# Kernel optimization log

Hardware: AMD Instinct MI355X
Metric: run time of the kernel (lower is better)

The kernel has to match this reference:

```python
import jax, jax.numpy as jnp
import numpy as np

B, S, H = 2, 2048, 2048
NH, NKV, HD = 16, 8, 128        # head_dim = H // NH
WINDOW = 1024                    # sliding window size
THETA = 100000.0                 # rope_theta (RotaryEmbedding base)


def setup_inputs() -> dict:
    key = jax.random.key(0)
    ks = jax.random.split(key, 5)
    hidden = jax.random.normal(ks[0], (B, S, H), jnp.float32)
    # fused QKV projection: [H, NH*HD + 2*NKV*HD]
    W_pack = jax.random.normal(ks[1], (H, NH * HD + 2 * NKV * HD), jnp.float32) * (H ** -0.5)
    W_o = jax.random.normal(ks[2], (NH * HD, H), jnp.float32) * ((NH * HD) ** -0.5)
    # per-KV-head 2-tap causal conv weights, softmax-normalized (as in nn.Parameter init)
    conv_k = jax.nn.softmax(jax.random.normal(ks[3], (NKV, 2), jnp.float32), axis=-1)
    conv_v = jax.nn.softmax(jax.random.normal(ks[4], (NKV, 2), jnp.float32), axis=-1)
    return {"hidden": hidden, "W_pack": W_pack, "W_o": W_o, "conv_k": conv_k, "conv_v": conv_v}


def _rope(x, cos, sin):
    # x: (b, s, h, d); cos/sin: (s, d//2); non-interleaved (rotate-half) form
    d2 = x.shape[-1] // 2
    x1, x2 = x[..., :d2], x[..., d2:]
    c = cos[None, :, None, :]
    s = sin[None, :, None, :]
    return jnp.concatenate([x1 * c - x2 * s, x2 * c + x1 * s], axis=-1)


def _causal_conv2(x, w):
    # x: (b, s, kv, d); w: (kv, 2). out[t] = w0*x[t-1] + w1*x[t], zero-padded at t=0
    x_prev = jnp.pad(x, ((0, 0), (1, 0), (0, 0), (0, 0)))[:, :-1]
    return w[None, None, :, 0:1] * x_prev + w[None, None, :, 1:2] * x


def reference(hidden, W_pack, W_o, conv_k, conv_v):
    b, s, _ = hidden.shape
    qkv = hidden @ W_pack                                  # (b, s, NH*HD + 2*NKV*HD)
    q = qkv[..., : NH * HD].reshape(b, s, NH, HD)
    k = qkv[..., NH * HD : NH * HD + NKV * HD].reshape(b, s, NKV, HD)
    v = qkv[..., NH * HD + NKV * HD :].reshape(b, s, NKV, HD)

    inv_freq = 1.0 / (THETA ** (jnp.arange(0, HD, 2, dtype=jnp.float32) / HD))
    freqs = jnp.outer(jnp.arange(s, dtype=jnp.float32), inv_freq)  # (s, HD/2)
    cos, sin = jnp.cos(freqs), jnp.sin(freqs)
    q = _rope(q, cos, sin)
    k = _rope(k, cos, sin)

    # learned 2-tap causal conv mixing adjacent K/V states, per KV head
    k = _causal_conv2(k, conv_k)
    v = _causal_conv2(v, conv_v)

    # GQA: repeat kv heads to match query heads
    group = NH // NKV
    k = jnp.repeat(k, group, axis=2)  # (b, s, NH, HD)
    v = jnp.repeat(v, group, axis=2)

    scores = jnp.einsum('bqhd,bkhd->bhqk', q, k) / jnp.sqrt(jnp.float32(HD))
    i = jnp.arange(s)[:, None]
    j = jnp.arange(s)[None, :]
    mask = (j <= i) & (i - j < WINDOW)  # causal sliding-window mask
    scores = jnp.where(mask[None, None], scores, jnp.finfo(scores.dtype).min)
    probs = jax.nn.softmax(scores, axis=-1)
    out = jnp.einsum('bhqk,bkhd->bqhd', probs, v).reshape(b, s, NH * HD)
    return out @ W_o
```

## Files before the change

### kernel.cpp

```cpp
#include <hip/hip_runtime.h>

#define DI __device__ __forceinline__

typedef unsigned short u16;
typedef __attribute__((ext_vector_type(8))) short s16x8;
typedef __attribute__((ext_vector_type(8))) unsigned short u16x8;
typedef __attribute__((ext_vector_type(4))) float f32x4;
typedef __attribute__((ext_vector_type(16))) float f32x16;

DI u16 f2bf(float x) {
  union { float f; unsigned u; } a; a.f = x;
  unsigned r = a.u + 0x7FFFu + ((a.u >> 16) & 1u);
  return (u16)(r >> 16);
}
DI float bf2f(u16 u) {
  union { unsigned u; float f; } a; a.u = ((unsigned)u) << 16;
  return a.f;
}
DI void gload16(const void* g, void* l) {
  __builtin_amdgcn_global_load_lds(
      (const __attribute__((address_space(1))) unsigned int*)g,
      (__attribute__((address_space(3))) unsigned int*)l, 16, 0, 0);
}
DI f32x4 mfma16(s16x8 a, s16x8 b, f32x4 c) {
  return __builtin_amdgcn_mfma_f32_16x16x32_bf16(a, b, c, 0, 0, 0);
}
DI f32x16 mfma32(s16x8 a, s16x8 b, f32x16 c) {
  return __builtin_amdgcn_mfma_f32_32x32x16_bf16(a, b, c, 0, 0, 0);
}

DI void store_out(float* p, float v) { *p = v; }
DI void store_out(u16* p, float v) { *p = f2bf(v); }

#define SBAR() asm volatile("s_barrier" ::: "memory")
#define WAIT_LGKM0() do { asm volatile("s_waitcnt lgkmcnt(0)" ::: "memory"); \
                          __builtin_amdgcn_sched_barrier(0); } while (0)

__global__ void cvt_kernel(const float* __restrict__ in, u16* __restrict__ out, int n8) {
  int i = blockIdx.x * 256 + threadIdx.x;
  if (i >= n8) return;
  const float4* p = (const float4*)in + (size_t)i * 2;
  float4 a = p[0], b = p[1];
  u16x8 o;
  o[0] = f2bf(a.x); o[1] = f2bf(a.y); o[2] = f2bf(a.z); o[3] = f2bf(a.w);
  o[4] = f2bf(b.x); o[5] = f2bf(b.y); o[6] = f2bf(b.z); o[7] = f2bf(b.w);
  *((u16x8*)out + i) = o;
}

__global__ void cvt_t_kernel(const float* __restrict__ W, u16* __restrict__ Wt, int R, int C) {
  __shared__ u16 tile[64][65];
  int c0 = blockIdx.x * 64, r0 = blockIdx.y * 64;
  int t = threadIdx.x;
#pragma unroll
  for (int i = 0; i < 16; ++i) {
    int flat = i * 256 + t;
    int r = flat >> 6, c = flat & 63;
    tile[r][c] = f2bf(W[(size_t)(r0 + r) * C + (c0 + c)]);
  }
  __syncthreads();
#pragma unroll
  for (int i = 0; i < 16; ++i) {
    int flat = i * 256 + t;
    int c = flat >> 6, r = flat & 63;
    Wt[(size_t)(c0 + c) * R + (r0 + r)] = tile[r][c];
  }
}

__global__ void rope_table_kernel(float* __restrict__ cosT, float* __restrict__ sinT) {
  int i = blockIdx.x * 256 + threadIdx.x;
  int s = i >> 6, d = i & 63;
  float inv = expf(-(float)d * (11.5129254649702295f / 64.f));
  float f = (float)s * inv;
  cosT[i] = cosf(f);
  sinT[i] = sinf(f);
}

template <typename OutT>
__global__ __launch_bounds__(512, 2) void gemm8p_kernel(
    const u16* __restrict__ A, const u16* __restrict__ Bt, OutT* __restrict__ C,
    int M, int N, int K) {
  __shared__ __align__(16) char lds[131072];
  int nwg = gridDim.x;
  int bid = blockIdx.x;
  int cpx = nwg >> 3;
  int swz = (bid & 7) * cpx + (bid >> 3);
  int ntn = N >> 8;
  int bm = swz / ntn, bn = swz - bm * ntn;
  int m0 = bm << 8, n0 = bn << 8;
  int t = threadIdx.x, w = t >> 6, l = t & 63;
  int wm = w >> 2, wn = w & 3;
  int NT = K >> 6;

  unsigned offA[2][2], offB[2][2];
  int cA[2][2], cB[2][2];
#pragma unroll
  for (int h = 0; h < 2; ++h)
#pragma unroll
    for (int i = 0; i < 2; ++i) {
      int c = i * 16 + h * 8 + w;
      cA[h][i] = c;
      int d = c * 1024 + l * 16;
      int s = d ^ (((d >> 9) & 1) << 5);
      offA[h][i] = (unsigned)(m0 + (s >> 7)) * (unsigned)(K * 2) + (unsigned)(s & 127);
      int c2 = ((w >> 2) << 3) + (w & 3) + h * 4 + i * 16;
      cB[h][i] = c2;
      int d2 = c2 * 1024 + l * 16;
      int s2 = d2 ^ (((d2 >> 9) & 1) << 5);
      offB[h][i] = (unsigned)(n0 + (s2 >> 7)) * (unsigned)(K * 2) + (unsigned)(s2 & 127);
    }
  const char* Ab = (const char*)A;
  const char* Bb = (const char*)Bt;

#define STAGE_A(tile, h) do { int _t = (tile); if (_t < NT) {                  \
    unsigned _k = (unsigned)_t * 128u;                                          \
    char* _ba = lds + ((_t & 1) << 16);                                         \
    gload16(Ab + (size_t)(offA[h][0] + _k), _ba + cA[h][0] * 1024);             \
    gload16(Ab + (size_t)(offA[h][1] + _k), _ba + cA[h][1] * 1024); } } while (0)
#define STAGE_B(tile, h) do { int _t = (tile); if (_t < NT) {                  \
    unsigned _k = (unsigned)_t * 128u;                                          \
    char* _bb = lds + ((_t & 1) << 16) + 32768;                                 \
    gload16(Bb + (size_t)(offB[h][0] + _k), _bb + cB[h][0] * 1024);             \
    gload16(Bb + (size_t)(offB[h][1] + _k), _bb + cB[h][1] * 1024); } } while (0)

  int lanemix = (((l & 15) << 7) + ((l >> 4) << 4)) ^ ((l & 4) << 3);

  f32x4 acc[8][4] = {};
  s16x8 af[4][2], b0f[2][2], b1f[2][2];

  STAGE_A(0, 0); STAGE_B(0, 0); STAGE_A(0, 1); STAGE_B(0, 1);
  STAGE_A(1, 0); STAGE_B(1, 0); STAGE_A(1, 1);
  asm volatile("s_waitcnt vmcnt(6)" ::: "memory");
  SBAR();

  for (int tt = 0; tt < NT; ++tt) {
    const char* ldsA = lds + ((tt & 1) << 16);
    const char* ldsB = ldsA + 32768;
    const char* Ard = ldsA + (wm << 14) + lanemix;
    const char* Brd = ldsB + (wn << 13) + lanemix;

#pragma unroll
    for (int mf = 0; mf < 4; ++mf) {
      af[mf][0] = *(const s16x8*)(Ard + mf * 2048);
      af[mf][1] = *(const s16x8*)(Ard + mf * 2048 + 64);
    }
#pragma unroll
    for (int nf = 0; nf < 2; ++nf) {
      b0f[nf][0] = *(const s16x8*)(Brd + nf * 2048);
      b0f[nf][1] = *(const s16x8*)(Brd + nf * 2048 + 64);
    }
    STAGE_B(tt + 1, 1);
    SBAR();
    WAIT_LGKM0();
    __builtin_amdgcn_s_setprio(1);
#pragma unroll
    for (int mf = 0; mf < 4; ++mf)
#pragma unroll
      for (int nf = 0; nf < 2; ++nf) {
        acc[mf][nf] = mfma16(af[mf][0], b0f[nf][0], acc[mf][nf]);
        acc[mf][nf] = mfma16(af[mf][1], b0f[nf][1], acc[mf][nf]);
      }
    __builtin_amdgcn_s_setprio(0);
    SBAR();

#pragma unroll
    for (int nf = 0; nf < 2; ++nf) {
      b1f[nf][0] = *(const s16x8*)(Brd + (nf + 2) * 2048);
      b1f[nf][1] = *(const s16x8*)(Brd + (nf + 2) * 2048 + 64);
    }
    STAGE_A(tt + 2, 0);
    SBAR();
    WAIT_LGKM0();
    __builtin_amdgcn_s_setprio(1);
#pragma unroll
    for (int mf = 0; mf < 4; ++mf)
#pragma unroll
      for (int nf = 0; nf < 2; ++nf) {
        acc[mf][nf + 2] = mfma16(af[mf][0], b1f[nf][0], acc[mf][nf + 2]);
        acc[mf][nf + 2] = mfma16(af[mf][1], b1f[nf][1], acc[mf][nf + 2]);
      }
    __builtin_amdgcn_s_setprio(0);
    SBAR();

#pragma unroll
    for (int mf = 0; mf < 4; ++mf) {
      af[mf][0] = *(const s16x8*)(Ard + (mf + 4) * 2048);
      af[mf][1] = *(const s16x8*)(Ard + (mf + 4) * 2048 + 64);
    }
    STAGE_B(tt + 2, 0);
    SBAR();
    WAIT_LGKM0();
    __builtin_amdgcn_s_setprio(1);
#pragma unroll
    for (int mf = 0; mf < 4; ++mf)
#pragma unroll
      for (int nf = 0; nf < 2; ++nf) {
        acc[mf + 4][nf] = mfma16(af[mf][0], b0f[nf][0], acc[mf + 4][nf]);
        acc[mf + 4][nf] = mfma16(af[mf][1], b0f[nf][1], acc[mf + 4][nf]);
      }
    __builtin_amdgcn_s_setprio(0);
    SBAR();

    STAGE_A(tt + 2, 1);
    SBAR();
    WAIT_LGKM0();
    __builtin_amdgcn_s_setprio(1);
#pragma unroll
    for (int mf = 0; mf < 4; ++mf)
#pragma unroll
      for (int nf = 0; nf < 2; ++nf) {
        acc[mf + 4][nf + 2] = mfma16(af[mf][0], b1f[nf][0], acc[mf + 4][nf + 2]);
        acc[mf + 4][nf + 2] = mfma16(af[mf][1], b1f[nf][1], acc[mf + 4][nf + 2]);
      }
    __builtin_amdgcn_s_setprio(0);
    if (tt < NT - 2) asm volatile("s_waitcnt vmcnt(6)" ::: "memory");
    else             asm volatile("s_waitcnt vmcnt(0)" ::: "memory");
    SBAR();
  }
#undef STAGE_A
#undef STAGE_B

#pragma unroll
  for (int mf = 0; mf < 8; ++mf)
#pragma unroll
    for (int nf = 0; nf < 4; ++nf) {
      int col = n0 + wn * 64 + nf * 16 + (l & 15);
#pragma unroll
      for (int j = 0; j < 4; ++j) {
        int row = m0 + wm * 128 + mf * 16 + (l >> 4) * 4 + j;
        store_out(C + (size_t)row * N + col, acc[mf][nf][j]);
      }
    }
}

__global__ void ropeconv_kernel(const u16* __restrict__ qkv, const float* __restrict__ cosT,
                                const float* __restrict__ sinT, const float* __restrict__ convk,
                                u16* __restrict__ qb, u16* __restrict__ kb) {
  const float qs = 0.08838834764831845f;
  int row = blockIdx.x;
  int b = row >> 11, s = row & 2047;
  int t = threadIdx.x;
  const u16* qr = qkv + (size_t)row * 4096;
  u16* qo = qb + (size_t)row * 2048;
#pragma unroll
  for (int i = 0; i < 4; ++i) {
    int p = i * 256 + t;
    int h = p >> 6, d = p & 63;
    float x1 = bf2f(qr[h * 128 + d]), x2 = bf2f(qr[h * 128 + 64 + d]);
    float c = cosT[s * 64 + d], sn = sinT[s * 64 + d];
    qo[h * 128 + d] = f2bf((x1 * c - x2 * sn) * qs);
    qo[h * 128 + 64 + d] = f2bf((x2 * c + x1 * sn) * qs);
  }
  const u16* kr = qr + 2048;
#pragma unroll
  for (int i = 0; i < 2; ++i) {
    int p = i * 256 + t;
    int h = p >> 6, d = p & 63;
    float c = cosT[s * 64 + d], sn = sinT[s * 64 + d];
    float x1 = bf2f(kr[h * 128 + d]), x2 = bf2f(kr[h * 128 + 64 + d]);
    float r1 = x1 * c - x2 * sn, r2 = x2 * c + x1 * sn;
    float p1 = 0.f, p2 = 0.f;
    if (s > 0) {
      const u16* kp = kr - 4096;
      float cp = cosT[(s - 1) * 64 + d], sp = sinT[(s - 1) * 64 + d];
      float y1 = bf2f(kp[h * 128 + d]), y2 = bf2f(kp[h * 128 + 64 + d]);
      p1 = y1 * cp - y2 * sp;
      p2 = y2 * cp + y1 * sp;
    }
    float w0 = convk[h * 2], w1 = convk[h * 2 + 1];
    size_t o = (((size_t)b * 8 + h) * 2048 + s) * 128;
    kb[o + d] = f2bf(w0 * p1 + w1 * r1);
    kb[o + 64 + d] = f2bf(w0 * p2 + w1 * r2);
  }
}

__global__ void vtrans_kernel(const u16* __restrict__ qkv, const float* __restrict__ convv,
                              u16* __restrict__ vt) {
  __shared__ u16 lt[128][72];
  int st = blockIdx.x, bh = blockIdx.y;
  int b = bh >> 3, h = bh & 7;
  int s0 = st * 64;
  int t = threadIdx.x;
  float w0 = convv[h * 2], w1 = convv[h * 2 + 1];
#pragma unroll
  for (int i = 0; i < 32; ++i) {
    int flat = i * 256 + t;
    int sl = flat >> 7, d = flat & 127;
    int s = s0 + sl;
    int row = b * 2048 + s;
    float x = bf2f(qkv[(size_t)row * 4096 + 3072 + h * 128 + d]);
    float xp = (s > 0) ? bf2f(qkv[(size_t)(row - 1) * 4096 + 3072 + h * 128 + d]) : 0.f;
    lt[d][sl] = f2bf(w0 * xp + w1 * x);
  }
  __syncthreads();
#pragma unroll
  for (int i = 0; i < 32; ++i) {
    int flat = i * 256 + t;
    int d = flat >> 6, sl = flat & 63;
    vt[((size_t)(b * 8 + h) * 128 + d) * 2048 + s0 + sl] = lt[d][sl];
  }
}

__global__ __launch_bounds__(256, 2) void attn2_kernel(
    const u16* __restrict__ qb, const u16* __restrict__ kbuf, const u16* __restrict__ vt,
    u16* __restrict__ ao) {
  __shared__ __align__(16) char lds[65536];
  int qt = blockIdx.x, bh = blockIdx.y;
  int b = bh >> 4, h = bh & 15, kh = h >> 1;
  int t = threadIdx.x, w = t >> 6, l = t & 63;
  int i0 = qt * 128;
  int qbase = i0 + w * 32;
  int lq = l & 31, hi = l >> 5;
  int xorc = (l & 7) << 4;
  const char* Kg = (const char*)(kbuf + (size_t)(b * 8 + kh) * 2048 * 128);
  const char* Vg = (const char*)(vt + (size_t)(b * 8 + kh) * 128 * 2048);

  s16x8 qf[8];
  {
    const u16* qp = qb + ((size_t)(b * 2048 + qbase + lq)) * 2048 + h * 128 + 8 * hi;
#pragma unroll
    for (int kc = 0; kc < 8; ++kc) qf[kc] = *(const s16x8*)(qp + kc * 16);
  }

  unsigned ksrc[4], vsrc[4], kdst[4], vdst[4];
#pragma unroll
  for (int i = 0; i < 4; ++i) {
    int c = w * 4 + i;
    int row = c * 4 + (l >> 4);
    int colb = (l & 15) * 16;
    ksrc[i] = (unsigned)(row * 256 + (colb ^ ((row & 7) << 4)));
    kdst[i] = (unsigned)(c * 1024);
    int d = c * 8 + (l >> 3);
    int cb2 = (l & 7) * 16;
    vsrc[i] = (unsigned)(d * 4096 + (cb2 ^ ((d & 7) << 4)));
    vdst[i] = (unsigned)(16384 + c * 1024);
  }

#define STAGEKV(tile, buf) do { int _j2 = (tile) << 6;                          \
    char* _lb = lds + ((buf) << 15);                                             \
    const char* _ks = Kg + (size_t)_j2 * 256;                                    \
    const char* _vs = Vg + (size_t)_j2 * 2;                                      \
    gload16(_ks + ksrc[0], _lb + kdst[0]); gload16(_vs + vsrc[0], _lb + vdst[0]);\
    gload16(_ks + ksrc[1], _lb + kdst[1]); gload16(_vs + vsrc[1], _lb + vdst[1]);\
    gload16(_ks + ksrc[2], _lb + kdst[2]); gload16(_vs + vsrc[2], _lb + vdst[2]);\
    gload16(_ks + ksrc[3], _lb + kdst[3]); gload16(_vs + vsrc[3], _lb + vdst[3]);\
  } while (0)

  int lo = i0 - 1023; if (lo < 0) lo = 0;
  int tk0 = lo >> 6, tk1 = (i0 + 127) >> 6;

  f32x16 acco[4] = {};
  float ls0 = 0.f, ls1 = 0.f, ls2 = 0.f, ls3 = 0.f;

  int cur = 0;
  STAGEKV(tk0, 0);
  asm volatile("s_waitcnt vmcnt(0)" ::: "memory");
  SBAR();

  for (int tk = tk0; tk <= tk1; ++tk) {
    int j0 = tk << 6;
    if (tk < tk1) STAGEKV(tk + 1, cur ^ 1);
    bool relevant = (j0 <= qbase + 31) && (j0 + 63 >= qbase - 1023);
    if (relevant) {
      const char* Kl = lds + (cur << 15);
      const char* Vl = Kl + 16384;
      const char* Krow = Kl + lq * 256;
      f32x16 ps0 = {}, ps1 = {};
      __builtin_amdgcn_s_setprio(1);
#pragma unroll
      for (int kc = 0; kc < 8; ++kc) {
        s16x8 kf = *(const s16x8*)(Krow + ((kc * 32 + hi * 16) ^ xorc));
        ps0 = mfma32(kf, qf[kc], ps0);
      }
#pragma unroll
      for (int kc = 0; kc < 8; ++kc) {
        s16x8 kf = *(const s16x8*)(Krow + 8192 + ((kc * 32 + hi * 16) ^ xorc));
        ps1 = mfma32(kf, qf[kc], ps1);
      }
      __builtin_amdgcn_s_setprio(0);
      bool domask = (j0 + 63 > qbase) || (qbase + 31 - j0 >= 1024);
      int di0 = qbase + lq - j0;
      float pe[32];
#pragma unroll
      for (int r = 0; r < 16; ++r) {
        float s0 = ps0[r], s1 = ps1[r];
        if (domask) {
          int crow = (r & 3) + 8 * (r >> 2) + 4 * hi;
          if ((unsigned)(di0 - crow) >= 1024u) s0 = -1e30f;
          if ((unsigned)(di0 - 32 - crow) >= 1024u) s1 = -1e30f;
        }
        float e0 = __expf(s0), e1 = __expf(s1);
        pe[r] = e0; pe[16 + r] = e1;
        if ((r & 3) == 0) { ls0 += e0 + e1; }
        else if ((r & 3) == 1) { ls1 += e0 + e1; }
        else if ((r & 3) == 2) { ls2 += e0 + e1; }
        else { ls3 += e0 + e1; }
      }
      unsigned pk[16];
#pragma unroll
      for (int p = 0; p < 16; ++p) {
        asm("v_cvt_pk_bf16_f32 %0, %1, %2" : "=v"(pk[p]) : "v"(pe[2 * p]), "v"(pe[2 * p + 1]));
      }
      s16x8 pa[4];
#pragma unroll
      for (int ks = 0; ks < 4; ++ks) {
        int base = (ks >> 1) * 8 + (ks & 1) * 4;
        unsigned keep0 = hi ? pk[base + 2] : pk[base + 0];
        unsigned keep1 = hi ? pk[base + 3] : pk[base + 1];
        unsigned send0 = hi ? pk[base + 0] : pk[base + 2];
        unsigned send1 = hi ? pk[base + 1] : pk[base + 3];
        unsigned recv0 = (unsigned)__shfl_xor((int)send0, 32);
        unsigned recv1 = (unsigned)__shfl_xor((int)send1, 32);
        union { unsigned u[4]; s16x8 v; } pu;
        pu.u[0] = hi ? recv0 : keep0;
        pu.u[1] = hi ? recv1 : keep1;
        pu.u[2] = hi ? keep0 : recv0;
        pu.u[3] = hi ? keep1 : recv1;
        pa[ks] = pu.v;
      }
      __builtin_amdgcn_s_setprio(1);
#pragma unroll
      for (int db = 0; db < 4; ++db) {
        const char* Vrow = Vl + db * 4096 + lq * 128;
#pragma unroll
        for (int ks = 0; ks < 4; ++ks) {
          s16x8 vf = *(const s16x8*)(Vrow + ((ks * 32 + hi * 16) ^ xorc));
          acco[db] = mfma32(pa[ks], vf, acco[db]);
        }
      }
      __builtin_amdgcn_s_setprio(0);
    }
    asm volatile("s_waitcnt vmcnt(0)" ::: "memory");
    SBAR();
    cur ^= 1;
  }
#undef STAGEKV

  float lrow = (ls0 + ls1) + (ls2 + ls3);
  float lt2 = lrow + __shfl_xor(lrow, 32);
  float rinv = 1.f / lt2;
#pragma unroll
  for (int r = 0; r < 16; ++r) {
    int qidx = (r & 3) + 8 * (r >> 2) + 4 * hi;
    float rv = __shfl(rinv, qidx);
    int i = qbase + qidx;
    u16* orow = ao + ((size_t)(b * 2048 + i)) * 2048 + h * 128 + lq;
#pragma unroll
    for (int db = 0; db < 4; ++db)
      orow[db * 32] = f2bf(acco[db][r] * rv);
  }
}

extern "C" void kernel_launch(void* const* d_in, const int* in_sizes, int n_in,
                              void* d_out, int out_size, void* d_ws, size_t ws_size,
                              hipStream_t stream) {
  (void)in_sizes; (void)n_in; (void)out_size; (void)ws_size;
  const float* hidden = (const float*)d_in[0];
  const float* W_pack = (const float*)d_in[1];
  const float* W_o    = (const float*)d_in[2];
  const float* conv_k = (const float*)d_in[3];
  const float* conv_v = (const float*)d_in[4];

  char* ws = (char*)d_ws;
  const size_t MB = 1u << 20;
  u16* hA    = (u16*)(ws + 0);
  u16* wpT   = (u16*)(ws + 16 * MB);
  u16* woT   = (u16*)(ws + 32 * MB);
  u16* qkv   = (u16*)(ws + 40 * MB);
  u16* qb    = (u16*)(ws + 72 * MB);
  u16* kbuf  = (u16*)(ws + 88 * MB);
  u16* vtb   = (u16*)(ws + 96 * MB);
  float* cosT = (float*)(ws + 104 * MB);
  float* sinT = (float*)(ws + 104 * MB + 524288);
  u16* attnb = qkv;

  cvt_kernel<<<4096, 256, 0, stream>>>(hidden, hA, 1048576);
  cvt_t_kernel<<<dim3(64, 32), 256, 0, stream>>>(W_pack, wpT, 2048, 4096);
  cvt_t_kernel<<<dim3(32, 32), 256, 0, stream>>>(W_o, woT, 2048, 2048);
  rope_table_kernel<<<512, 256, 0, stream>>>(cosT, sinT);
  gemm8p_kernel<u16><<<256, 512, 0, stream>>>(hA, wpT, qkv, 4096, 4096, 2048);
  ropeconv_kernel<<<4096, 256, 0, stream>>>(qkv, cosT, sinT, conv_k, qb, kbuf);
  vtrans_kernel<<<dim3(32, 16), 256, 0, stream>>>(qkv, conv_v, vtb);
  attn2_kernel<<<dim3(16, 32), 256, 0, stream>>>(qb, kbuf, vtb, attnb);
  gemm8p_kernel<float><<<128, 512, 0, stream>>>(attnb, woT, (float*)d_out,
                                                4096, 2048, 2048);
}
```

Baseline: 229.2 us.

## Use 256x128 tile GEMM for output projection and full 8-way LDS swizzle

Adds a new GEMM kernel with a 256x128 output tile for the output projection, so it launches 256 workgroups instead of 128 and fills more compute units. The kernel uses 2-per-CU launch bounds with a 96KB LDS double buffer. It also changes the LDS XOR swizzle in both GEMMs from a 1-bit to a 3-bit row-based pattern, with matching read-side lane offsets, to reduce bank conflicts. The trade-off is lower per-tile reuse of A in the smaller tile.

```diff
diff --git a/kernel.cpp b/kernel.cpp
--- a/kernel.cpp
+++ b/kernel.cpp
@@ -100,12 +100,12 @@
       int c = i * 16 + h * 8 + w;
       cA[h][i] = c;
       int d = c * 1024 + l * 16;
-      int s = d ^ (((d >> 9) & 1) << 5);
+      int s = d ^ ((((d >> 7) & 7)) << 4);
       offA[h][i] = (unsigned)(m0 + (s >> 7)) * (unsigned)(K * 2) + (unsigned)(s & 127);
       int c2 = ((w >> 2) << 3) + (w & 3) + h * 4 + i * 16;
       cB[h][i] = c2;
       int d2 = c2 * 1024 + l * 16;
-      int s2 = d2 ^ (((d2 >> 9) & 1) << 5);
+      int s2 = d2 ^ ((((d2 >> 7) & 7)) << 4);
       offB[h][i] = (unsigned)(n0 + (s2 >> 7)) * (unsigned)(K * 2) + (unsigned)(s2 & 127);
     }
   const char* Ab = (const char*)A;
@@ -122,7 +122,8 @@
     gload16(Bb + (size_t)(offB[h][0] + _k), _bb + cB[h][0] * 1024);             \
     gload16(Bb + (size_t)(offB[h][1] + _k), _bb + cB[h][1] * 1024); } } while (0)
 
-  int lanemix = (((l & 15) << 7) + ((l >> 4) << 4)) ^ ((l & 4) << 3);
+  int lanemix = ((l & 15) << 7) + ((((l >> 4) << 4) ^ ((l & 7) << 4)));
+  int lanemix1 = lanemix ^ 64;
 
   f32x4 acc[8][4] = {};
   s16x8 af[4][2], b0f[2][2], b1f[2][2];
@@ -135,18 +136,20 @@
   for (int tt = 0; tt < NT; ++tt) {
     const char* ldsA = lds + ((tt & 1) << 16);
     const char* ldsB = ldsA + 32768;
-    const char* Ard = ldsA + (wm << 14) + lanemix;
-    const char* Brd = ldsB + (wn << 13) + lanemix;
-
-#pragma unroll
-    for (int mf = 0; mf < 4; ++mf) {
-      af[mf][0] = *(const s16x8*)(Ard + mf * 2048);
-      af[mf][1] = *(const s16x8*)(Ard + mf * 2048 + 64);
+    const char* Ard0 = ldsA + (wm << 14) + lanemix;
+    const char* Ard1 = ldsA + (wm << 14) + lanemix1;
+    const char* Brd0 = ldsB + (wn << 13) + lanemix;
+    const char* Brd1 = ldsB + (wn << 13) + lanemix1;
+
+#pragma unroll
+    for (int mf = 0; mf < 4; ++mf) {
+      af[mf][0] = *(const s16x8*)(Ard0 + mf * 2048);
+      af[mf][1] = *(const s16x8*)(Ard1 + mf * 2048);
     }
 #pragma unroll
     for (int nf = 0; nf < 2; ++nf) {
-      b0f[nf][0] = *(const s16x8*)(Brd + nf * 2048);
-      b0f[nf][1] = *(const s16x8*)(Brd + nf * 2048 + 64);
+      b0f[nf][0] = *(const s16x8*)(Brd0 + nf * 2048);
+      b0f[nf][1] = *(const s16x8*)(Brd1 + nf * 2048);
     }
     STAGE_B(tt + 1, 1);
     SBAR();
@@ -164,8 +167,8 @@
 
 #pragma unroll
     for (int nf = 0; nf < 2; ++nf) {
-      b1f[nf][0] = *(const s16x8*)(Brd + (nf + 2) * 2048);
-      b1f[nf][1] = *(const s16x8*)(Brd + (nf + 2) * 2048 + 64);
+      b1f[nf][0] = *(const s16x8*)(Brd0 + (nf + 2) * 2048);
+      b1f[nf][1] = *(const s16x8*)(Brd1 + (nf + 2) * 2048);
     }
     STAGE_A(tt + 2, 0);
     SBAR();
@@ -183,8 +186,8 @@
 
 #pragma unroll
     for (int mf = 0; mf < 4; ++mf) {
-      af[mf][0] = *(const s16x8*)(Ard + (mf + 4) * 2048);
-      af[mf][1] = *(const s16x8*)(Ard + (mf + 4) * 2048 + 64);
+      af[mf][0] = *(const s16x8*)(Ard0 + (mf + 4) * 2048);
+      af[mf][1] = *(const s16x8*)(Ard1 + (mf + 4) * 2048);
     }
     STAGE_B(tt + 2, 0);
     SBAR();
@@ -228,6 +231,147 @@
       for (int j = 0; j < 4; ++j) {
         int row = m0 + wm * 128 + mf * 16 + (l >> 4) * 4 + j;
         store_out(C + (size_t)row * N + col, acc[mf][nf][j]);
+      }
+    }
+}
+
+__global__ __launch_bounds__(512, 2) void gemm8pn_kernel(
+    const u16* __restrict__ A, const u16* __restrict__ Bt, float* __restrict__ C,
+    int M, int N, int K) {
+  __shared__ __align__(16) char lds[98304];
+  int nwg = gridDim.x;
+  int bid = blockIdx.x;
+  int cpx = nwg >> 3;
+  int swz = (bid & 7) * cpx + (bid >> 3);
+  int ntn = N >> 7;
+  int bm = swz / ntn, bn = swz - bm * ntn;
+  int m0 = bm << 8, n0 = bn << 7;
+  int t = threadIdx.x, w = t >> 6, l = t & 63;
+  int wm = w >> 2, wn = w & 3;
+  int NT = K >> 6;
+
+  unsigned offA[4], offB[2];
+  int cA[4], cB[2];
+#pragma unroll
+  for (int u = 0; u < 4; ++u) {
+    int c = u * 8 + w;
+    cA[u] = c;
+    int d = c * 1024 + l * 16;
+    int s = d ^ ((((d >> 7) & 7)) << 4);
+    offA[u] = (unsigned)(m0 + (s >> 7)) * (unsigned)(K * 2) + (unsigned)(s & 127);
+  }
+#pragma unroll
+  for (int u = 0; u < 2; ++u) {
+    int c = u * 8 + w;
+    cB[u] = c;
+    int d = c * 1024 + l * 16;
+    int s = d ^ ((((d >> 7) & 7)) << 4);
+    offB[u] = (unsigned)(n0 + (s >> 7)) * (unsigned)(K * 2) + (unsigned)(s & 127);
+  }
+  const char* Ab = (const char*)A;
+  const char* Bb = (const char*)Bt;
+
+#define STG_A(tile, u) do { int _t = (tile); if (_t < NT) {                    \
+    gload16(Ab + (size_t)(offA[u] + (unsigned)_t * 128u),                       \
+            lds + (_t & 1) * 49152 + cA[u] * 1024); } } while (0)
+#define STG_B(tile, u) do { int _t = (tile); if (_t < NT) {                    \
+    gload16(Bb + (size_t)(offB[u] + (unsigned)_t * 128u),                       \
+            lds + (_t & 1) * 49152 + 32768 + cB[u] * 1024); } } while (0)
+
+  int lanemix = ((l & 15) << 7) + ((((l >> 4) << 4) ^ ((l & 7) << 4)));
+  int lanemix1 = lanemix ^ 64;
+
+  f32x4 acc[8][2] = {};
+  s16x8 af[4][2], bf0[2], bf1[2];
+
+  STG_A(0, 0); STG_A(0, 1); STG_A(0, 2); STG_A(0, 3); STG_B(0, 0); STG_B(0, 1);
+  STG_A(1, 0); STG_A(1, 1); STG_A(1, 2); STG_A(1, 3); STG_B(1, 0); STG_B(1, 1);
+  asm volatile("s_waitcnt vmcnt(6)" ::: "memory");
+  SBAR();
+
+  for (int tt = 0; tt < NT; ++tt) {
+    const char* ldsA = lds + (tt & 1) * 49152;
+    const char* ldsB = ldsA + 32768;
+    const char* Ard0 = ldsA + (wm << 14) + lanemix;
+    const char* Ard1 = ldsA + (wm << 14) + lanemix1;
+    const char* Brd0 = ldsB + (wn << 12) + lanemix;
+    const char* Brd1 = ldsB + (wn << 12) + lanemix1;
+
+#pragma unroll
+    for (int mf = 0; mf < 4; ++mf) {
+      af[mf][0] = *(const s16x8*)(Ard0 + mf * 2048);
+      af[mf][1] = *(const s16x8*)(Ard1 + mf * 2048);
+    }
+    bf0[0] = *(const s16x8*)(Brd0);
+    bf0[1] = *(const s16x8*)(Brd1);
+    SBAR();
+    WAIT_LGKM0();
+    __builtin_amdgcn_s_setprio(1);
+#pragma unroll
+    for (int mf = 0; mf < 4; ++mf) {
+      acc[mf][0] = mfma16(af[mf][0], bf0[0], acc[mf][0]);
+      acc[mf][0] = mfma16(af[mf][1], bf0[1], acc[mf][0]);
+    }
+    __builtin_amdgcn_s_setprio(0);
+    SBAR();
+
+    bf1[0] = *(const s16x8*)(Brd0 + 2048);
+    bf1[1] = *(const s16x8*)(Brd1 + 2048);
+    STG_A(tt + 2, 0); STG_A(tt + 2, 2);
+    SBAR();
+    WAIT_LGKM0();
+    __builtin_amdgcn_s_setprio(1);
+#pragma unroll
+    for (int mf = 0; mf < 4; ++mf) {
+      acc[mf][1] = mfma16(af[mf][0], bf1[0], acc[mf][1]);
+      acc[mf][1] = mfma16(af[mf][1], bf1[1], acc[mf][1]);
+    }
+    __builtin_amdgcn_s_setprio(0);
+    SBAR();
+
+#pragma unroll
+    for (int mf = 0; mf < 4; ++mf) {
+      af[mf][0] = *(const s16x8*)(Ard0 + (mf + 4) * 2048);
+      af[mf][1] = *(const s16x8*)(Ard1 + (mf + 4) * 2048);
+    }
+    STG_B(tt + 2, 0); STG_B(tt + 2, 1);
+    SBAR();
+    WAIT_LGKM0();
+    __builtin_amdgcn_s_setprio(1);
+#pragma unroll
+    for (int mf = 0; mf < 4; ++mf) {
+      acc[mf + 4][0] = mfma16(af[mf][0], bf0[0], acc[mf + 4][0]);
+      acc[mf + 4][0] = mfma16(af[mf][1], bf0[1], acc[mf + 4][0]);
+    }
+    __builtin_amdgcn_s_setprio(0);
+    SBAR();
+
+    STG_A(tt + 2, 1); STG_A(tt + 2, 3);
+    SBAR();
+    WAIT_LGKM0();
+    __builtin_amdgcn_s_setprio(1);
+#pragma unroll
+    for (int mf = 0; mf < 4; ++mf) {
+      acc[mf + 4][1] = mfma16(af[mf][0], bf1[0], acc[mf + 4][1]);
+      acc[mf + 4][1] = mfma16(af[mf][1], bf1[1], acc[mf + 4][1]);
+    }
+    __builtin_amdgcn_s_setprio(0);
+    if (tt < NT - 2) asm volatile("s_waitcnt vmcnt(6)" ::: "memory");
+    else             asm volatile("s_waitcnt vmcnt(0)" ::: "memory");
+    SBAR();
+  }
+#undef STG_A
+#undef STG_B
+
+#pragma unroll
+  for (int mf = 0; mf < 8; ++mf)
+#pragma unroll
+    for (int nf = 0; nf < 2; ++nf) {
+      int col = n0 + wn * 32 + nf * 16 + (l & 15);
+#pragma unroll
+      for (int j = 0; j < 4; ++j) {
+        int row = m0 + wm * 128 + mf * 16 + (l >> 4) * 4 + j;
+        C[(size_t)row * N + col] = acc[mf][nf][j];
       }
     }
 }
@@ -481,6 +625,6 @@
   ropeconv_kernel<<<4096, 256, 0, stream>>>(qkv, cosT, sinT, conv_k, qb, kbuf);
   vtrans_kernel<<<dim3(32, 16), 256, 0, stream>>>(qkv, conv_v, vtb);
   attn2_kernel<<<dim3(16, 32), 256, 0, stream>>>(qb, kbuf, vtb, attnb);
-  gemm8p_kernel<float><<<128, 512, 0, stream>>>(attnb, woT, (float*)d_out,
-                                                4096, 2048, 2048);
-}
+  gemm8pn_kernel<<<256, 512, 0, stream>>>(attnb, woT, (float*)d_out,
+                                          4096, 2048, 2048);
+}
```

Measured after the change: 203.9 us. -11.1%, faster.
